# Performance work log

Measured on AMD Instinct MI355X. Metric: run time of the kernel, lower is better.

## Reference

```python
import jax, jax.numpy as jnp
import numpy as np

NUM_HEADS = 16
HIDDEN = 1024
B, S = 2, 2048


def setup_inputs() -> dict:
    key = jax.random.key(0)
    ks = jax.random.split(key, 14)
    D = HIDDEN
    scale = 1.0 / np.sqrt(D)
    inp = {
        "query": jax.random.normal(ks[0], (B, S, D), jnp.float32),
        "key_in": jax.random.normal(ks[1], (B, S, D), jnp.float32),
        "value": jax.random.normal(ks[2], (B, S, D), jnp.float32),
        "group_prob": jax.random.uniform(ks[3], (B, S, S), jnp.float32),
        "mask": jax.random.randint(ks[4], (B, S, S), 0, 2, jnp.int32),
        "wq_k": jax.random.normal(ks[5], (D, D), jnp.float32) * scale,
        "wq_b": jnp.zeros((D,), jnp.float32),
        "wk_k": jax.random.normal(ks[6], (D, D), jnp.float32) * scale,
        "wk_b": jnp.zeros((D,), jnp.float32),
        "wv_k": jax.random.normal(ks[7], (D, D), jnp.float32) * scale,
        "wv_b": jnp.zeros((D,), jnp.float32),
        "wo_k": jax.random.normal(ks[8], (D, D), jnp.float32) * scale,
        "wo_b": jnp.zeros((D,), jnp.float32),
    }
    return inp


def _split_heads(x, H):
    b, s, d = x.shape
    return x.reshape(b, s, H, d // H).transpose(0, 2, 1, 3)  # (B,H,S,dh)


def reference(query, key_in, value, group_prob, mask,
              wq_k, wq_b, wk_k, wk_b, wv_k, wv_b, wo_k, wo_b):
    H = NUM_HEADS
    dh = query.shape[-1] // H
    q = _split_heads(query @ wq_k + wq_b, H)
    k = _split_heads(key_in @ wk_k + wk_b, H)
    v = _split_heads(value @ wv_k + wv_b, H)
    # scaled dot-product logits (B,H,Sq,Sk)
    logits = jnp.einsum('bhqd,bhkd->bhqk', q, k) / jnp.sqrt(jnp.asarray(dh, q.dtype))
    neg = (1.0 - mask.astype(q.dtype)) * -1e9
    logits = logits + neg[:, None, :, :]
    attn = jax.nn.softmax(logits, axis=-1)
    # Tree Transformer modulation: post-softmax elementwise scale by group_prob
    attn = attn * group_prob[:, None, :, :]
    out = jnp.einsum('bhqk,bhkd->bhqd', attn, v)
    out = out.transpose(0, 2, 1, 3).reshape(query.shape[0], -1, H * dh)
    return out @ wo_k + wo_b
```

## Files before the change

### kernel.cpp

```cpp
#include <hip/hip_runtime.h>
#include <hip/hip_bf16.h>
#include <stdint.h>

#define B_ 2
#define S_ 2048
#define D_ 1024
#define H_ 16
#define DH 64

typedef __attribute__((ext_vector_type(4))) float f32x4;
typedef __attribute__((ext_vector_type(8))) short s16x8;
typedef __attribute__((ext_vector_type(4))) short s16x4;

__device__ inline short f2bf(float f) {
  union { float f; unsigned u; } v; v.f = f;
  unsigned r = (v.u + 0x7fffu + ((v.u >> 16) & 1u)) >> 16;
  return (short)r;
}

__device__ inline float bfbits_lo(unsigned u) {
  union { unsigned x; float f; } v; v.x = u << 16; return v.f;
}
__device__ inline float bfbits_hi(unsigned u) {
  union { unsigned x; float f; } v; v.x = u & 0xffff0000u; return v.f;
}

__device__ inline float exp2v(float x) {
  float r; asm("v_exp_f32 %0, %1" : "=v"(r) : "v"(x)); return r;
}
__device__ inline unsigned cvtpk(float a, float b) {
  unsigned r; asm("v_cvt_pk_bf16_f32 %0, %1, %2" : "=v"(r) : "v"(a), "v"(b));
  return r;
}

__global__ __launch_bounds__(256) void cvt3_f32_bf16(const float* __restrict__ a,
                                                     const float* __restrict__ b,
                                                     const float* __restrict__ c,
                                                     short* oa, short* ob, short* oc,
                                                     int n) {
  int z = blockIdx.y;
  const float* in = z == 0 ? a : (z == 1 ? b : c);
  short* out = z == 0 ? oa : (z == 1 ? ob : oc);
  int i = (blockIdx.x * 256 + threadIdx.x) * 4;
  if (i < n) {
    float4 v = *(const float4*)(in + i);
    s16x4 o;
    o.x = f2bf(v.x); o.y = f2bf(v.y); o.z = f2bf(v.z); o.w = f2bf(v.w);
    *(s16x4*)(out + i) = o;
  }
}

__global__ __launch_bounds__(256) void fuse_mgp(const int* __restrict__ mask,
                                                const float* __restrict__ gp,
                                                short* __restrict__ mgp, int n) {
  int i = (blockIdx.x * 256 + threadIdx.x) * 4;
  if (i < n) {
    int4 m = *(const int4*)(mask + i);
    float4 g = *(const float4*)(gp + i);
    short b0 = f2bf(g.x); if (!b0) b0 = (short)0x0080;
    short b1 = f2bf(g.y); if (!b1) b1 = (short)0x0080;
    short b2 = f2bf(g.z); if (!b2) b2 = (short)0x0080;
    short b3 = f2bf(g.w); if (!b3) b3 = (short)0x0080;
    s16x4 o;
    o.x = m.x ? b0 : 0;
    o.y = m.y ? b1 : 0;
    o.z = m.z ? b2 : 0;
    o.w = m.w ? b3 : 0;
    *(s16x4*)(mgp + i) = o;
  }
}

__global__ __launch_bounds__(256) void transpose_cvt4(
    const float* __restrict__ i0, const float* __restrict__ i1,
    const float* __restrict__ i2, const float* __restrict__ i3,
    short* o0, short* o1, short* o2, short* o3) {
  int z = blockIdx.z;
  const float* in = z == 0 ? i0 : (z == 1 ? i1 : (z == 2 ? i2 : i3));
  short* out = z == 0 ? o0 : (z == 1 ? o1 : (z == 2 ? o2 : o3));
  __shared__ float tile[32][33];
  int bx = blockIdx.x, by = blockIdx.y;
  int x = bx * 32 + threadIdx.x;
#pragma unroll
  for (int i = 0; i < 32; i += 8) {
    int y = by * 32 + threadIdx.y + i;
    tile[threadIdx.y + i][threadIdx.x] = in[(size_t)y * D_ + x];
  }
  __syncthreads();
  int ox = by * 32 + threadIdx.x;
#pragma unroll
  for (int i = 0; i < 32; i += 8) {
    int oy = bx * 32 + threadIdx.y + i;
    out[(size_t)oy * D_ + ox] = f2bf(tile[threadIdx.x][threadIdx.y + i]);
  }
}

__global__ __launch_bounds__(256) void transpose_v(const short* __restrict__ vp,
                                                   short* __restrict__ vt) {
  __shared__ __align__(16) short t[64 * 72];
  int tid = threadIdx.x;
  int bh = blockIdx.y, b = bh >> 4, h = bh & 15;
  int s0 = blockIdx.x * 64;
  int r = tid >> 2, cc = tid & 3;
  const short* src = vp + ((size_t)(b * S_ + s0 + r)) * D_ + h * DH + cc * 16;
  s16x8 a = *(const s16x8*)src;
  s16x8 bb = *(const s16x8*)(src + 8);
  int pc = (cc ^ (r >> 4)) * 16;
  *(s16x8*)&t[r * 72 + pc] = a;
  *(s16x8*)&t[r * 72 + pc + 8] = bb;
  __syncthreads();
  int d = tid >> 2, sc = (tid & 3) * 16;
  s16x8 o0, o1;
#pragma unroll
  for (int j = 0; j < 8; ++j) {
    int row = sc + j;
    o0[j] = t[row * 72 + ((d >> 4) ^ (row >> 4)) * 16 + (d & 15)];
    int row2 = sc + 8 + j;
    o1[j] = t[row2 * 72 + ((d >> 4) ^ (row2 >> 4)) * 16 + (d & 15)];
  }
  short* dst = vt + ((size_t)(b * H_ + h) * DH + d) * S_ + s0 + sc;
  *(s16x8*)dst = o0;
  *(s16x8*)(dst + 8) = o1;
}

__device__ inline void gload_lds16(const void* g, void* l) {
  __builtin_amdgcn_global_load_lds(
      (const __attribute__((address_space(1))) unsigned*)g,
      (__attribute__((address_space(3))) unsigned*)l, 16, 0, 0);
}

#define BM 128
#define BN 128
#define BK 32

__global__ __launch_bounds__(256) void gemm_bt3(
    const short* __restrict__ A0, const short* __restrict__ A1, const short* __restrict__ A2,
    const short* __restrict__ Bt0, const short* __restrict__ Bt1, const short* __restrict__ Bt2,
    const float* __restrict__ bs0, const float* __restrict__ bs1, const float* __restrict__ bs2,
    void* C0, void* C1, void* C2,
    int M, int N, int K, int f32out, float os0, float os1, float os2) {
  int z = blockIdx.y;
  const short* A = z == 0 ? A0 : (z == 1 ? A1 : A2);
  const short* Bt = z == 0 ? Bt0 : (z == 1 ? Bt1 : Bt2);
  const float* bias = z == 0 ? bs0 : (z == 1 ? bs1 : bs2);
  void* C = z == 0 ? C0 : (z == 1 ? C1 : C2);
  float oscale = z == 0 ? os0 : (z == 1 ? os1 : os2);

  __shared__ __align__(16) short As[BM * BK];
  __shared__ __align__(16) short Bs[BN * BK];
  int tid = threadIdx.x;
  int lane = tid & 63, wave = tid >> 6;
  int l15 = lane & 15, l4 = lane >> 4;
  int ntn = N / BN;
  int bm = blockIdx.x / ntn, bn = blockIdx.x % ntn;
  int row0 = bm * BM, col0 = bn * BN;
  int wm = (wave >> 1) * 64, wn = (wave & 1) * 64;

  f32x4 acc[4][4] = {};

  for (int k0 = 0; k0 < K; k0 += BK) {
    __syncthreads();
#pragma unroll
    for (int it = 0; it < 2; ++it) {
      int ch = it * 256 + tid;
      int r = ch >> 2, c = (ch & 3) * 8;
      int ldsbase = (it * 256 + wave * 64) * 8;
      gload_lds16(A + (size_t)(row0 + r) * K + k0 + c, &As[ldsbase]);
      gload_lds16(Bt + (size_t)(col0 + r) * K + k0 + c, &Bs[ldsbase]);
    }
    __syncthreads();
    s16x8 af[4], bf[4];
#pragma unroll
    for (int mf = 0; mf < 4; ++mf)
      af[mf] = *(const s16x8*)&As[(wm + mf * 16 + l15) * BK + l4 * 8];
#pragma unroll
    for (int nf = 0; nf < 4; ++nf)
      bf[nf] = *(const s16x8*)&Bs[(wn + nf * 16 + l15) * BK + l4 * 8];
#pragma unroll
    for (int mf = 0; mf < 4; ++mf)
#pragma unroll
      for (int nf = 0; nf < 4; ++nf)
        acc[mf][nf] = __builtin_amdgcn_mfma_f32_16x16x32_bf16(af[mf], bf[nf],
                                                              acc[mf][nf], 0, 0, 0);
  }

#pragma unroll
  for (int nf = 0; nf < 4; ++nf) {
    int gcol = col0 + wn + nf * 16 + l15;
    float bv = bias[gcol];
#pragma unroll
    for (int mf = 0; mf < 4; ++mf) {
#pragma unroll
      for (int r = 0; r < 4; ++r) {
        int grow = row0 + wm + mf * 16 + l4 * 4 + r;
        float v = (acc[mf][nf][r] + bv) * oscale;
        if (f32out)
          ((float*)C)[(size_t)grow * N + gcol] = v;
        else
          ((short*)C)[(size_t)grow * N + gcol] = f2bf(v);
      }
    }
  }
}

#define QB 128
#define NB 64
#define NTILES (S_ / NB)
#define M0_SHIFT 12.0f

__global__ __launch_bounds__(256, 3) void attn_fused(const short* __restrict__ Qp,
                                                     const short* __restrict__ Kp,
                                                     const short* __restrict__ VT,
                                                     const short* __restrict__ MGP,
                                                     short* __restrict__ ctx) {
  __shared__ __align__(16) short Ks[2][64 * 64];
  __shared__ __align__(16) short Vs[2][64 * 64];
  __shared__ __align__(16) short Ps[4][32 * 64];

  int tid = threadIdx.x, lane = tid & 63, wave = tid >> 6;
  int l15 = lane & 15, l4 = lane >> 4;
  int q0 = blockIdx.x * QB;
  int bh = blockIdx.y;
  int b = bh >> 4, h = bh & 15;
  int wq = wave * 32;

  const short* Qbase = Qp + (size_t)b * S_ * D_ + (size_t)h * DH;
  const short* Kbase = Kp + (size_t)b * S_ * D_ + (size_t)h * DH;
  const short* Vbase = VT + (size_t)(b * H_ + h) * DH * S_;
  const short* Mrow0 = MGP + (size_t)b * S_ * S_ + (size_t)(q0 + wq + l15) * S_ + l4 * 4;
  const short* Mrow1 = Mrow0 + (size_t)16 * S_;

  int i0 = tid, i1 = 256 + tid;
  int r0 = i0 >> 3, c0 = (i0 & 7) ^ (r0 & 7);
  int r1 = i1 >> 3, c1 = (i1 & 7) ^ (r1 & 7);
  int ldsA = wave * 512;
  int ldsB = 2048 + wave * 512;

#define STAGE(kv0, buf)                                                       \
  do {                                                                        \
    gload_lds16(Kbase + (size_t)((kv0) + r0) * D_ + c0 * 8, &Ks[buf][ldsA]);  \
    gload_lds16(Kbase + (size_t)((kv0) + r1) * D_ + c1 * 8, &Ks[buf][ldsB]);  \
    gload_lds16(Vbase + (size_t)r0 * S_ + (kv0) + c0 * 8, &Vs[buf][ldsA]);    \
    gload_lds16(Vbase + (size_t)r1 * S_ + (kv0) + c1 * 8, &Vs[buf][ldsB]);    \
  } while (0)

  s16x8 qf[2][2];
#pragma unroll
  for (int mf = 0; mf < 2; ++mf)
#pragma unroll
    for (int ks = 0; ks < 2; ++ks)
      qf[mf][ks] = *(const s16x8*)(Qbase + (size_t)(q0 + wq + mf * 16 + l15) * D_ +
                                   ks * 32 + l4 * 8);

  float lsum[2] = {0.f, 0.f};
  f32x4 oacc[2][4] = {};

  STAGE(0, 0);

  int q7 = l15 & 7;
  short* Pw = &Ps[wave][0];
  int prow[2] = {l15 * 64, (16 + l15) * 64};

  for (int t = 0; t < NTILES; ++t) {
    int buf = t & 1;
    int kvt = t * NB;

    uint2 g2[2][4];
#pragma unroll
    for (int nf = 0; nf < 4; ++nf) {
      g2[0][nf] = *(const uint2*)(Mrow0 + kvt + nf * 16);
      g2[1][nf] = *(const uint2*)(Mrow1 + kvt + nf * 16);
    }
    __builtin_amdgcn_sched_barrier(0);
    if (t + 1 < NTILES) {
      STAGE((t + 1) * NB, buf ^ 1);
      __builtin_amdgcn_sched_barrier(0);
      asm volatile("s_waitcnt vmcnt(12)" ::: "memory");
    } else {
      __builtin_amdgcn_sched_barrier(0);
      asm volatile("s_waitcnt vmcnt(8)" ::: "memory");
    }
    __builtin_amdgcn_s_barrier();
    __builtin_amdgcn_sched_barrier(0);

    f32x4 sacc[2][4] = {};
#pragma unroll
    for (int nf = 0; nf < 4; ++nf) {
      int R = nf * 16 + l15;
#pragma unroll
      for (int ks = 0; ks < 2; ++ks) {
        s16x8 kf = *(const s16x8*)&Ks[buf][R * 64 + (((ks * 4 + l4) ^ q7) * 8)];
#pragma unroll
        for (int mf = 0; mf < 2; ++mf)
          sacc[mf][nf] = __builtin_amdgcn_mfma_f32_16x16x32_bf16(kf, qf[mf][ks],
                                                                 sacc[mf][nf], 0, 0, 0);
      }
    }

    if (t + 1 < NTILES)
      asm volatile("s_waitcnt vmcnt(4)" ::: "memory");
    else
      asm volatile("s_waitcnt vmcnt(0)" ::: "memory");
    __builtin_amdgcn_sched_barrier(0);

#pragma unroll
    for (int mf = 0; mf < 2; ++mf) {
#pragma unroll
      for (int nf = 0; nf < 4; ++nf) {
        float gv0 = bfbits_lo(g2[mf][nf].x), gv1 = bfbits_hi(g2[mf][nf].x);
        float gv2 = bfbits_lo(g2[mf][nf].y), gv3 = bfbits_hi(g2[mf][nf].y);
        float e0 = exp2v(sacc[mf][nf][0] - M0_SHIFT);
        float e1 = exp2v(sacc[mf][nf][1] - M0_SHIFT);
        float e2 = exp2v(sacc[mf][nf][2] - M0_SHIFT);
        float e3 = exp2v(sacc[mf][nf][3] - M0_SHIFT);
        lsum[mf] += (gv0 != 0.f) ? e0 : 0.f;
        lsum[mf] += (gv1 != 0.f) ? e1 : 0.f;
        lsum[mf] += (gv2 != 0.f) ? e2 : 0.f;
        lsum[mf] += (gv3 != 0.f) ? e3 : 0.f;
        uint2 wp;
        wp.x = cvtpk(e0 * gv0, e1 * gv1);
        wp.y = cvtpk(e2 * gv2, e3 * gv3);
        int gr = ((nf * 2 + (l4 >> 1)) ^ q7) * 8 + (l4 & 1) * 4;
        *(uint2*)&Pw[prow[mf] + gr] = wp;
      }
    }

#pragma unroll
    for (int ks = 0; ks < 2; ++ks) {
      s16x8 pa[2];
#pragma unroll
      for (int mf = 0; mf < 2; ++mf)
        pa[mf] = *(const s16x8*)&Pw[prow[mf] + (((ks * 4 + l4) ^ q7) * 8)];
#pragma unroll
      for (int df = 0; df < 4; ++df) {
        s16x8 vf = *(const s16x8*)&Vs[buf][(df * 16 + l15) * 64 +
                                           (((ks * 4 + l4) ^ q7) * 8)];
#pragma unroll
        for (int mf = 0; mf < 2; ++mf)
          oacc[mf][df] = __builtin_amdgcn_mfma_f32_16x16x32_bf16(vf, pa[mf],
                                                                 oacc[mf][df], 0, 0, 0);
      }
    }

    asm volatile("s_waitcnt lgkmcnt(0)" ::: "memory");
    __builtin_amdgcn_s_barrier();
  }
#undef STAGE

#pragma unroll
  for (int mf = 0; mf < 2; ++mf) {
    float ls = lsum[mf];
    ls += __shfl_xor(ls, 16);
    ls += __shfl_xor(ls, 32);
    float inv = 1.f / ls;
    short* crow = ctx + ((size_t)(b * S_ + q0 + wq + mf * 16 + l15)) * D_ + h * DH;
#pragma unroll
    for (int df = 0; df < 4; ++df) {
      uint2 o;
      o.x = cvtpk(oacc[mf][df][0] * inv, oacc[mf][df][1] * inv);
      o.y = cvtpk(oacc[mf][df][2] * inv, oacc[mf][df][3] * inv);
      *(uint2*)(crow + df * 16 + l4 * 4) = o;
    }
  }
}

extern "C" void kernel_launch(void* const* d_in, const int* in_sizes, int n_in,
                              void* d_out, int out_size, void* d_ws, size_t ws_size,
                              hipStream_t stream) {
  const float* query = (const float*)d_in[0];
  const float* key_in = (const float*)d_in[1];
  const float* value = (const float*)d_in[2];
  const float* group_prob = (const float*)d_in[3];
  const int* mask = (const int*)d_in[4];
  const float* wq_k = (const float*)d_in[5];
  const float* wq_b = (const float*)d_in[6];
  const float* wk_k = (const float*)d_in[7];
  const float* wk_b = (const float*)d_in[8];
  const float* wv_k = (const float*)d_in[9];
  const float* wv_b = (const float*)d_in[10];
  const float* wo_k = (const float*)d_in[11];
  const float* wo_b = (const float*)d_in[12];
  float* out = (float*)d_out;

  short* ws = (short*)d_ws;
  const size_t NT = (size_t)B_ * S_ * D_;
  short* qbf = ws;
  short* kbf = qbf + NT;
  short* vbf = kbf + NT;
  short* wqt = vbf + NT;
  short* wkt = wqt + (size_t)D_ * D_;
  short* wvt = wkt + (size_t)D_ * D_;
  short* wot = wvt + (size_t)D_ * D_;
  short* qp = wot + (size_t)D_ * D_;
  short* kp = qp + NT;
  short* vp = kp + NT;
  short* ctx = vp + NT;
  short* mgp = ws;
  short* vt = vbf;

  int nblk = (int)(NT / 4 / 256);
  cvt3_f32_bf16<<<dim3(nblk, 3), 256, 0, stream>>>(query, key_in, value,
                                                   qbf, kbf, vbf, (int)NT);

  dim3 tb(32, 8);
  transpose_cvt4<<<dim3(D_ / 32, D_ / 32, 4), tb, 0, stream>>>(
      wq_k, wk_k, wv_k, wo_k, wqt, wkt, wvt, wot);

  int M = B_ * S_;
  int gblocks = (M / BM) * (D_ / BN);
  const float QSCALE = 0.125f * 1.4426950408889634f;
  gemm_bt3<<<dim3(gblocks, 3), 256, 0, stream>>>(
      qbf, kbf, vbf, wqt, wkt, wvt, wq_b, wk_b, wv_b, qp, kp, vp,
      M, D_, D_, 0, QSCALE, 1.0f, 1.0f);

  int nmg = B_ * S_ * S_;
  fuse_mgp<<<nmg / 4 / 256, 256, 0, stream>>>(mask, group_prob, mgp, nmg);
  transpose_v<<<dim3(S_ / 64, B_ * H_), 256, 0, stream>>>(vp, vt);

  dim3 ag(S_ / QB, B_ * H_);
  attn_fused<<<ag, 256, 0, stream>>>(qp, kp, vt, mgp, ctx);

  gemm_bt3<<<dim3(gblocks, 1), 256, 0, stream>>>(
      ctx, ctx, ctx, wot, wot, wot, wo_b, wo_b, wo_b, out, out, out,
      M, D_, D_, 1, 1.0f, 1.0f, 1.0f);
}
```

Baseline: 188.0 us.

## Triple-buffer K/V tiles and prefetch mask/group-prob one tile ahead

```diff
diff --git a/kernel.cpp b/kernel.cpp
--- a/kernel.cpp
+++ b/kernel.cpp
@@ -207,13 +207,13 @@
 #define NTILES (S_ / NB)
 #define M0_SHIFT 12.0f
 
-__global__ __launch_bounds__(256, 3) void attn_fused(const short* __restrict__ Qp,
+__global__ __launch_bounds__(256, 2) void attn_fused(const short* __restrict__ Qp,
                                                      const short* __restrict__ Kp,
                                                      const short* __restrict__ VT,
                                                      const short* __restrict__ MGP,
                                                      short* __restrict__ ctx) {
-  __shared__ __align__(16) short Ks[2][64 * 64];
-  __shared__ __align__(16) short Vs[2][64 * 64];
+  __shared__ __align__(16) short KsAll[3 * 64 * 64];
+  __shared__ __align__(16) short VsAll[3 * 64 * 64];
   __shared__ __align__(16) short Ps[4][32 * 64];
 
   int tid = threadIdx.x, lane = tid & 63, wave = tid >> 6;
@@ -235,12 +235,25 @@
   int ldsA = wave * 512;
   int ldsB = 2048 + wave * 512;
 
-#define STAGE(kv0, buf)                                                       \
+#define STAGE(tile, bi)                                                       \
   do {                                                                        \
-    gload_lds16(Kbase + (size_t)((kv0) + r0) * D_ + c0 * 8, &Ks[buf][ldsA]);  \
-    gload_lds16(Kbase + (size_t)((kv0) + r1) * D_ + c1 * 8, &Ks[buf][ldsB]);  \
-    gload_lds16(Vbase + (size_t)r0 * S_ + (kv0) + c0 * 8, &Vs[buf][ldsA]);    \
-    gload_lds16(Vbase + (size_t)r1 * S_ + (kv0) + c1 * 8, &Vs[buf][ldsB]);    \
+    int kvs = (tile) * NB;                                                    \
+    short* kd = &KsAll[(bi) * 4096];                                          \
+    short* vd = &VsAll[(bi) * 4096];                                          \
+    gload_lds16(Kbase + (size_t)(kvs + r0) * D_ + c0 * 8, kd + ldsA);         \
+    gload_lds16(Kbase + (size_t)(kvs + r1) * D_ + c1 * 8, kd + ldsB);         \
+    gload_lds16(Vbase + (size_t)r0 * S_ + kvs + c0 * 8, vd + ldsA);           \
+    gload_lds16(Vbase + (size_t)r1 * S_ + kvs + c1 * 8, vd + ldsB);           \
+  } while (0)
+
+#define LOADMGP(dst, tile)                                                    \
+  do {                                                                        \
+    int kvx = (tile) * NB;                                                    \
+    _Pragma("unroll")                                                         \
+    for (int nf = 0; nf < 4; ++nf) {                                          \
+      dst[0][nf] = *(const uint2*)(Mrow0 + kvx + nf * 16);                    \
+      dst[1][nf] = *(const uint2*)(Mrow1 + kvx + nf * 16);                    \
+    }                                                                         \
   } while (0)
 
   s16x8 qf[2][2];
@@ -253,98 +266,95 @@
 
   float lsum[2] = {0.f, 0.f};
   f32x4 oacc[2][4] = {};
-
-  STAGE(0, 0);
-
+  uint2 g2a[2][4], g2b[2][4];
+
+  int b0 = 0, b1 = 1, b2 = 2;
   int q7 = l15 & 7;
   short* Pw = &Ps[wave][0];
   int prow[2] = {l15 * 64, (16 + l15) * 64};
 
-  for (int t = 0; t < NTILES; ++t) {
-    int buf = t & 1;
-    int kvt = t * NB;
-
-    uint2 g2[2][4];
-#pragma unroll
-    for (int nf = 0; nf < 4; ++nf) {
-      g2[0][nf] = *(const uint2*)(Mrow0 + kvt + nf * 16);
-      g2[1][nf] = *(const uint2*)(Mrow1 + kvt + nf * 16);
-    }
-    __builtin_amdgcn_sched_barrier(0);
-    if (t + 1 < NTILES) {
-      STAGE((t + 1) * NB, buf ^ 1);
-      __builtin_amdgcn_sched_barrier(0);
-      asm volatile("s_waitcnt vmcnt(12)" ::: "memory");
-    } else {
-      __builtin_amdgcn_sched_barrier(0);
-      asm volatile("s_waitcnt vmcnt(8)" ::: "memory");
-    }
-    __builtin_amdgcn_s_barrier();
-    __builtin_amdgcn_sched_barrier(0);
-
-    f32x4 sacc[2][4] = {};
-#pragma unroll
-    for (int nf = 0; nf < 4; ++nf) {
-      int R = nf * 16 + l15;
-#pragma unroll
-      for (int ks = 0; ks < 2; ++ks) {
-        s16x8 kf = *(const s16x8*)&Ks[buf][R * 64 + (((ks * 4 + l4) ^ q7) * 8)];
-#pragma unroll
-        for (int mf = 0; mf < 2; ++mf)
-          sacc[mf][nf] = __builtin_amdgcn_mfma_f32_16x16x32_bf16(kf, qf[mf][ks],
-                                                                 sacc[mf][nf], 0, 0, 0);
-      }
-    }
-
-    if (t + 1 < NTILES)
-      asm volatile("s_waitcnt vmcnt(4)" ::: "memory");
-    else
-      asm volatile("s_waitcnt vmcnt(0)" ::: "memory");
-    __builtin_amdgcn_sched_barrier(0);
-
-#pragma unroll
-    for (int mf = 0; mf < 2; ++mf) {
-#pragma unroll
-      for (int nf = 0; nf < 4; ++nf) {
-        float gv0 = bfbits_lo(g2[mf][nf].x), gv1 = bfbits_hi(g2[mf][nf].x);
-        float gv2 = bfbits_lo(g2[mf][nf].y), gv3 = bfbits_hi(g2[mf][nf].y);
-        float e0 = exp2v(sacc[mf][nf][0] - M0_SHIFT);
-        float e1 = exp2v(sacc[mf][nf][1] - M0_SHIFT);
-        float e2 = exp2v(sacc[mf][nf][2] - M0_SHIFT);
-        float e3 = exp2v(sacc[mf][nf][3] - M0_SHIFT);
-        lsum[mf] += (gv0 != 0.f) ? e0 : 0.f;
-        lsum[mf] += (gv1 != 0.f) ? e1 : 0.f;
-        lsum[mf] += (gv2 != 0.f) ? e2 : 0.f;
-        lsum[mf] += (gv3 != 0.f) ? e3 : 0.f;
-        uint2 wp;
-        wp.x = cvtpk(e0 * gv0, e1 * gv1);
-        wp.y = cvtpk(e2 * gv2, e3 * gv3);
-        int gr = ((nf * 2 + (l4 >> 1)) ^ q7) * 8 + (l4 & 1) * 4;
-        *(uint2*)&Pw[prow[mf] + gr] = wp;
-      }
-    }
-
-#pragma unroll
-    for (int ks = 0; ks < 2; ++ks) {
-      s16x8 pa[2];
-#pragma unroll
-      for (int mf = 0; mf < 2; ++mf)
-        pa[mf] = *(const s16x8*)&Pw[prow[mf] + (((ks * 4 + l4) ^ q7) * 8)];
-#pragma unroll
-      for (int df = 0; df < 4; ++df) {
-        s16x8 vf = *(const s16x8*)&Vs[buf][(df * 16 + l15) * 64 +
-                                           (((ks * 4 + l4) ^ q7) * 8)];
-#pragma unroll
-        for (int mf = 0; mf < 2; ++mf)
-          oacc[mf][df] = __builtin_amdgcn_mfma_f32_16x16x32_bf16(vf, pa[mf],
-                                                                 oacc[mf][df], 0, 0, 0);
-      }
-    }
-
-    asm volatile("s_waitcnt lgkmcnt(0)" ::: "memory");
-    __builtin_amdgcn_s_barrier();
-  }
+  STAGE(0, 0);
+  __builtin_amdgcn_sched_barrier(0);
+  LOADMGP(g2a, 0);
+  __builtin_amdgcn_sched_barrier(0);
+  STAGE(1, 1);
+  __builtin_amdgcn_sched_barrier(0);
+
+#define TILE_BODY(t, CUR, NXT)                                                \
+  do {                                                                        \
+    LOADMGP(NXT, ((t) + 1) & (NTILES - 1));                                   \
+    __builtin_amdgcn_sched_barrier(0);                                        \
+    asm volatile("s_waitcnt vmcnt(20) lgkmcnt(0)" ::: "memory");              \
+    __builtin_amdgcn_s_barrier();                                             \
+    __builtin_amdgcn_sched_barrier(0);                                        \
+    STAGE(((t) + 2) & (NTILES - 1), b2);                                      \
+    __builtin_amdgcn_sched_barrier(0);                                        \
+    const short* Kb = &KsAll[b0 * 4096];                                      \
+    const short* Vb = &VsAll[b0 * 4096];                                      \
+    f32x4 sacc[2][4] = {};                                                    \
+    _Pragma("unroll")                                                         \
+    for (int nf = 0; nf < 4; ++nf) {                                          \
+      int R = nf * 16 + l15;                                                  \
+      _Pragma("unroll")                                                       \
+      for (int ks = 0; ks < 2; ++ks) {                                        \
+        s16x8 kf = *(const s16x8*)&Kb[R * 64 + (((ks * 4 + l4) ^ q7) * 8)];   \
+        _Pragma("unroll")                                                     \
+        for (int mf = 0; mf < 2; ++mf)                                        \
+          sacc[mf][nf] = __builtin_amdgcn_mfma_f32_16x16x32_bf16(             \
+              kf, qf[mf][ks], sacc[mf][nf], 0, 0, 0);                         \
+      }                                                                       \
+    }                                                                         \
+    asm volatile("s_waitcnt vmcnt(16)" ::: "memory");                         \
+    __builtin_amdgcn_sched_barrier(0);                                        \
+    _Pragma("unroll")                                                         \
+    for (int mf = 0; mf < 2; ++mf) {                                          \
+      _Pragma("unroll")                                                       \
+      for (int nf = 0; nf < 4; ++nf) {                                        \
+        float gv0 = bfbits_lo(CUR[mf][nf].x), gv1 = bfbits_hi(CUR[mf][nf].x); \
+        float gv2 = bfbits_lo(CUR[mf][nf].y), gv3 = bfbits_hi(CUR[mf][nf].y); \
+        float e0 = exp2v(sacc[mf][nf][0] - M0_SHIFT);                         \
+        float e1 = exp2v(sacc[mf][nf][1] - M0_SHIFT);                         \
+        float e2 = exp2v(sacc[mf][nf][2] - M0_SHIFT);                         \
+        float e3 = exp2v(sacc[mf][nf][3] - M0_SHIFT);                         \
+        lsum[mf] += (gv0 != 0.f) ? e0 : 0.f;                                  \
+        lsum[mf] += (gv1 != 0.f) ? e1 : 0.f;                                  \
+        lsum[mf] += (gv2 != 0.f) ? e2 : 0.f;                                  \
+        lsum[mf] += (gv3 != 0.f) ? e3 : 0.f;                                  \
+        uint2 wp;                                                             \
+        wp.x = cvtpk(e0 * gv0, e1 * gv1);                                     \
+        wp.y = cvtpk(e2 * gv2, e3 * gv3);                                     \
+        int gr = ((nf * 2 + (l4 >> 1)) ^ q7) * 8 + (l4 & 1) * 4;              \
+        *(uint2*)&Pw[prow[mf] + gr] = wp;                                     \
+      }                                                                       \
+    }                                                                         \
+    _Pragma("unroll")                                                         \
+    for (int ks = 0; ks < 2; ++ks) {                                          \
+      s16x8 pa[2];                                                            \
+      _Pragma("unroll")                                                       \
+      for (int mf = 0; mf < 2; ++mf)                                          \
+        pa[mf] = *(const s16x8*)&Pw[prow[mf] + (((ks * 4 + l4) ^ q7) * 8)];   \
+      _Pragma("unroll")                                                       \
+      for (int df = 0; df < 4; ++df) {                                        \
+        s16x8 vf = *(const s16x8*)&Vb[(df * 16 + l15) * 64 +                  \
+                                      (((ks * 4 + l4) ^ q7) * 8)];            \
+        _Pragma("unroll")                                                     \
+        for (int mf = 0; mf < 2; ++mf)                                        \
+          oacc[mf][df] = __builtin_amdgcn_mfma_f32_16x16x32_bf16(             \
+              vf, pa[mf], oacc[mf][df], 0, 0, 0);                             \
+      }                                                                       \
+    }                                                                         \
+    int _tmp = b0; b0 = b1; b1 = b2; b2 = _tmp;                               \
+  } while (0)
+
+  for (int t = 0; t < NTILES; t += 2) {
+    TILE_BODY(t, g2a, g2b);
+    TILE_BODY(t + 1, g2b, g2a);
+  }
+#undef TILE_BODY
 #undef STAGE
+#undef LOADMGP
+
+  asm volatile("s_waitcnt vmcnt(0) lgkmcnt(0)" ::: "memory");
 
 #pragma unroll
   for (int mf = 0; mf < 2; ++mf) {
```

After: 202.3 us. +7.6%, slower.
